# Performance work log

Measured on AMD Instinct MI355X. Metric: run time of the kernel, lower is better.

## Reference

```python
import jax, jax.numpy as jnp
import numpy as np

B, N, K, C, R = 2, 4096, 512, 384, 16
JITTER = 1e-4
W_ATTACH, W_ENTB = 1.0, 0.0


def overlap_score(delta, Sig):
    # fused_gaussian_overlap_score: bidirectional Mahalanobis overlap log-score
    # delta [..., 3], Sig [..., 3, 3] (SPD)
    sol = jnp.linalg.solve(Sig, delta[..., None])[..., 0]
    maha = (delta * sol).sum(-1)
    _, logdet = jnp.linalg.slogdet(Sig)
    return -0.5 * maha - 0.5 * logdet


def setup_inputs() -> dict:
    key = jax.random.key(0)
    ks = jax.random.split(key, 10)
    s_parent = jax.random.normal(ks[0], (B, K, C), jnp.float32)
    mu_parent = jax.random.normal(ks[1], (B, K, 3), jnp.float32) * 10.0
    A = jax.random.normal(ks[2], (B, K, 3, 3), jnp.float32)
    Sig_parent = A @ jnp.swapaxes(A, -1, -2) + 0.5 * jnp.eye(3, dtype=jnp.float32)
    mask_parent = jnp.ones((B, K), jnp.float32)
    node_mask = jnp.ones((B, N), jnp.float32)
    res_idx = jax.random.randint(ks[3], (B, N), 0, N)
    Bmat = jax.random.normal(ks[4], (1, C // 2), jnp.float32)  # Fourier freqs, scale=1.0
    Wq = jax.random.normal(ks[5], (C, C), jnp.float32) / np.sqrt(C).astype(np.float32)
    Wk = jax.random.normal(ks[6], (C, C), jnp.float32) / np.sqrt(C).astype(np.float32)
    Wv = jax.random.normal(ks[7], (C, C), jnp.float32) / np.sqrt(C).astype(np.float32)
    ln_g = jnp.ones((C,), jnp.float32)
    ln_b = jnp.zeros((C,), jnp.float32)
    return dict(s_parent=s_parent, mu_parent=mu_parent, Sig_parent=Sig_parent,
                mask_parent=mask_parent, node_mask=node_mask, res_idx=res_idx,
                Bmat=Bmat, Wq=Wq, Wk=Wk, Wv=Wv, ln_g=ln_g, ln_b=ln_b)


def reference(s_parent, mu_parent, Sig_parent, mask_parent, node_mask, res_idx,
              Bmat, Wq, Wk, Wv, ln_g, ln_b):
    eye3 = jnp.eye(3, dtype=s_parent.dtype)
    inv_sqrt_c = 1.0 / jnp.sqrt(jnp.asarray(C, s_parent.dtype))

    # --- ResIdxFourierEmbedding ---
    m = node_mask
    L = jnp.clip(m.sum(1, keepdims=True), 1.0)
    denom = jnp.clip(L - 1.0, 1.0)
    ri = jnp.clip(res_idx, 0, 4095).astype(s_parent.dtype)
    pos = jnp.clip(ri / denom, 0.0, 1.0)[..., None]                      # [B,N,1]
    proj = (2.0 * jnp.pi) * (pos @ Bmat)                                 # [B,N,C/2]
    emb = jnp.concatenate([jnp.cos(proj), jnp.sin(proj)], -1)            # [B,N,C]
    emb = emb * m[..., None]
    mu_e = emb.mean(-1, keepdims=True)
    var_e = ((emb - mu_e) ** 2).mean(-1, keepdims=True)
    q0 = (emb - mu_e) / jnp.sqrt(var_e + 1e-5) * ln_g + ln_b

    # --- routing projections ---
    q = q0 @ Wq                                                          # [B,N,C]
    k = s_parent @ Wk                                                    # [B,K,C]
    logits_full = jnp.einsum('bnc,bkc->bnk', q, k) * inv_sqrt_c
    logits_full = logits_full + (mask_parent[:, None, :] - 1.0) * 1e9
    j0 = jnp.argmax(logits_full, -1)                                     # [B,N]

    # --- topk parents by Gaussian overlap (no grad) ---
    mu_p = jax.lax.stop_gradient(mu_parent)
    Sig_p = jax.lax.stop_gradient(Sig_parent)
    delta_kk = mu_p[:, :, None, :] - mu_p[:, None, :, :]                 # [B,K,K,3]
    Sig_kk = Sig_p[:, :, None] + Sig_p[:, None, :] + 1e-6 * eye3         # [B,K,K,3,3]
    score_kk = overlap_score(delta_kk, Sig_kk)
    mask2d = mask_parent[:, None, :] * mask_parent[:, :, None]
    score_kk = jnp.where(mask2d < 0.5, -1e9, score_kk)
    knn = jax.lax.top_k(score_kk, R)[1]                                  # [B,K,R]
    parent_idx = knn[jnp.arange(B)[:, None], j0]                         # [B,N,R]

    # --- multi-level gathers ---
    gather = lambda tab: jax.vmap(lambda t, i: t[i])(tab, parent_idx)
    mu_sub = gather(mu_parent)                                           # [B,N,R,3]
    Sig_sub = gather(Sig_parent)                                         # [B,N,R,3,3]
    s_sub = gather(s_parent)                                             # [B,N,R,C]

    k_sub = s_sub @ Wk
    v_sub = s_sub @ Wv
    logits = (q[:, :, None, :] * k_sub).sum(-1) * inv_sqrt_c             # [B,N,R]
    logits = logits + (m[:, :, None] - 1.0) * 1e9
    B_local = jax.nn.softmax(logits, -1)

    s0 = jnp.einsum('bnr,bnrc->bnc', B_local, v_sub) * m[..., None]
    mu0 = jnp.einsum('bnr,bnrp->bnp', B_local, mu_sub)
    d = mu_sub - mu0[:, :, None, :]
    outer = d[..., :, None] * d[..., None, :]
    Sig0 = (B_local[..., None, None] * (Sig_sub + outer)).sum(2) + JITTER * eye3

    # --- geometric regularization ---
    delta0 = mu0[:, :, None, :] - mu_sub
    score = overlap_score(delta0, Sig_sub)                               # [B,N,R]
    dnm = jnp.clip(m.sum(), 1.0)
    loss_attach = -(m[:, :, None] * (B_local * score)).sum() / dnm
    ent = -(B_local * jnp.log(jnp.clip(B_local, 1e-9))).sum(-1)
    loss_ent_B = (ent * m).sum() / dnm

    occ = jax.vmap(lambda i, w: jnp.zeros((K,), w.dtype).at[i.reshape(-1)].add(w.reshape(-1)))(
        parent_idx, B_local * m[:, :, None])
    occ_norm = occ / jnp.clip(occ.sum(-1, keepdims=True), 1e-9)

    loss_geo = W_ATTACH * loss_attach + W_ENTB * loss_ent_B
    return s0, mu0, Sig0, B_local, occ_norm, loss_geo
```

## Files before the change

kernel.cpp:

```cpp
#include <hip/hip_runtime.h>
#include <math.h>

#define NB 2
#define NN 4096
#define NK 512
#define NC 384
#define NR 16
#define NCH 192
#define NSLICE 64

static constexpr float INV_SQRT_C = 0.051031036307982884f;
static constexpr float TWO_PI     = 6.283185307179586f;
static constexpr float F_JITTER   = 1e-4f;

typedef __attribute__((ext_vector_type(8))) short short8;
typedef __attribute__((ext_vector_type(4))) float f32x4;
typedef __attribute__((ext_vector_type(4))) unsigned short us4;
typedef __attribute__((ext_vector_type(8))) unsigned short us8;

__device__ __forceinline__ void split3(float x, unsigned short& h, unsigned short& m_, unsigned short& l_) {
    unsigned int xi = __float_as_uint(x);
    unsigned int uh = (xi + 0x7fffu + ((xi >> 16) & 1u)) >> 16;
    float fh = __uint_as_float(uh << 16);
    float r  = x - fh;
    unsigned int ri = __float_as_uint(r);
    unsigned int um = (ri + 0x7fffu + ((ri >> 16) & 1u)) >> 16;
    float fm = __uint_as_float(um << 16);
    float r2 = r - fm;
    unsigned int r2i = __float_as_uint(r2);
    unsigned int ul = (r2i + 0x7fffu + ((r2i >> 16) & 1u)) >> 16;
    h = (unsigned short)uh; m_ = (unsigned short)um; l_ = (unsigned short)ul;
}

__global__ __launch_bounds__(256) void k_pre(const float* __restrict__ node_mask,
                                             const float* __restrict__ Wk,
                                             const float* __restrict__ Wq,
                                             float* __restrict__ Lsum,
                                             float* __restrict__ W2) {
    __shared__ float red[256];
    __shared__ float As[16][68];
    __shared__ float Ws[16][68];
    int bid = blockIdx.x, t = threadIdx.x;
    if (bid < 2) {
        int b = bid;
        float s = 0.f;
        for (int n = t; n < NN; n += 256) s += node_mask[b*NN + n];
        red[t] = s; __syncthreads();
        for (int w = 128; w > 0; w >>= 1) { if (t < w) red[t] += red[t+w]; __syncthreads(); }
        if (t == 0) Lsum[b] = red[0];
        return;
    }
    int gb = bid - 2;
    int rowbase = (gb % 6) * 64, colbase = (gb / 6) * 64;
    int tx = t & 15, ty = t >> 4;
    float acc[4][4] = {};
    for (int k0 = 0; k0 < NC; k0 += 16) {
        {
            int r = t >> 2, ja = (t & 3) << 2;
            float4 a4 = *(const float4*)(Wk + (size_t)(rowbase + r)*NC + k0 + ja);
            As[ja+0][r] = a4.x; As[ja+1][r] = a4.y; As[ja+2][r] = a4.z; As[ja+3][r] = a4.w;
        }
        {
            int r = t >> 2, jb = (t & 3) << 2;
            float4 b4 = *(const float4*)(Wq + (size_t)(colbase + r)*NC + k0 + jb);
            Ws[jb+0][r] = b4.x; Ws[jb+1][r] = b4.y; Ws[jb+2][r] = b4.z; Ws[jb+3][r] = b4.w;
        }
        __syncthreads();
        #pragma unroll
        for (int kk = 0; kk < 16; ++kk) {
            float4 av = *(const float4*)&As[kk][ty<<2];
            float4 wv = *(const float4*)&Ws[kk][tx<<2];
            float aa[4] = {av.x, av.y, av.z, av.w};
            float ww[4] = {wv.x, wv.y, wv.z, wv.w};
            #pragma unroll
            for (int i = 0; i < 4; ++i)
                #pragma unroll
                for (int j = 0; j < 4; ++j)
                    acc[i][j] += aa[i]*ww[j];
        }
        __syncthreads();
    }
    #pragma unroll
    for (int i = 0; i < 4; ++i) {
        float4 o = make_float4(acc[i][0], acc[i][1], acc[i][2], acc[i][3]);
        *(float4*)(W2 + (size_t)(rowbase + (ty<<2) + i)*NC + colbase + (tx<<2)) = o;
    }
}

template<bool SPLIT>
__global__ __launch_bounds__(256) void k_mid(const float* __restrict__ s_parent,
                                             const float* __restrict__ Wv,
                                             const float* __restrict__ W2,
                                             const int* __restrict__ res_idx,
                                             const float* __restrict__ node_mask,
                                             const float* __restrict__ Bm,
                                             const float* __restrict__ ln_g,
                                             const float* __restrict__ ln_b,
                                             const float* __restrict__ Lsum,
                                             const float* __restrict__ mu,
                                             const float* __restrict__ Sg,
                                             const float* __restrict__ maskp,
                                             float* __restrict__ vmat,
                                             float* __restrict__ GtF,
                                             unsigned short* __restrict__ gh,
                                             unsigned short* __restrict__ gm,
                                             unsigned short* __restrict__ gl,
                                             float* __restrict__ q0f,
                                             unsigned short* __restrict__ qh,
                                             unsigned short* __restrict__ qm,
                                             unsigned short* __restrict__ ql,
                                             int* __restrict__ knn) {
    __shared__ float As[16][68];
    __shared__ float Ws[16][68];
    int bid = blockIdx.x, t = threadIdx.x;

    if (bid < 192) {
        int z = bid / 96, rem = bid % 96;
        int rowbase = (rem % 16) * 64, colbase = (rem / 16) * 64;
        const float* W = z ? W2 : Wv;
        int tx = t & 15, ty = t >> 4;
        float acc[4][4] = {};
        for (int k0 = 0; k0 < NC; k0 += 16) {
            {
                int r = t >> 2, ja = (t & 3) << 2;
                float4 a4 = *(const float4*)(s_parent + (size_t)(rowbase + r)*NC + k0 + ja);
                As[ja+0][r] = a4.x; As[ja+1][r] = a4.y; As[ja+2][r] = a4.z; As[ja+3][r] = a4.w;
            }
            {
                int kr = t >> 4, jw = (t & 15) << 2;
                float4 w4 = *(const float4*)(W + (size_t)(k0 + kr)*NC + colbase + jw);
                *(float4*)&Ws[kr][jw] = w4;
            }
            __syncthreads();
            #pragma unroll
            for (int kk = 0; kk < 16; ++kk) {
                float4 av = *(const float4*)&As[kk][ty<<2];
                float4 wv = *(const float4*)&Ws[kk][tx<<2];
                float aa[4] = {av.x, av.y, av.z, av.w};
                float ww[4] = {wv.x, wv.y, wv.z, wv.w};
                #pragma unroll
                for (int i = 0; i < 4; ++i)
                    #pragma unroll
                    for (int j = 0; j < 4; ++j)
                        acc[i][j] += aa[i]*ww[j];
            }
            __syncthreads();
        }
        #pragma unroll
        for (int i = 0; i < 4; ++i) {
            size_t ro = (size_t)(rowbase + (ty<<2) + i)*NC + colbase + (tx<<2);
            if (z == 0) {
                *(float4*)(vmat + ro) = make_float4(acc[i][0], acc[i][1], acc[i][2], acc[i][3]);
            } else if constexpr (SPLIT) {
                us4 vh, vm, vl;
                #pragma unroll
                for (int j = 0; j < 4; ++j) {
                    unsigned short h, mm, ll;
                    split3(acc[i][j], h, mm, ll);
                    vh[j] = h; vm[j] = mm; vl[j] = ll;
                }
                *(us4*)(gh + ro) = vh; *(us4*)(gm + ro) = vm; *(us4*)(gl + ro) = vl;
            } else {
                *(float4*)(GtF + ro) = make_float4(acc[i][0], acc[i][1], acc[i][2], acc[i][3]);
            }
        }
        return;
    }

    if (bid < 448) {
        int wv_ = t >> 6, lane = t & 63;
        int tb = ((bid - 192) << 2) + wv_;
        int b = tb >> 9, i = tb & 511;
        const float* mui = mu + (size_t)(b*NK + i)*3;
        const float* Sgi = Sg + (size_t)(b*NK + i)*9;
        float mi0 = mui[0], mi1 = mui[1], mi2 = mui[2];
        float S0 = Sgi[0], S1 = Sgi[1], S2 = Sgi[2], S4 = Sgi[4], S5 = Sgi[5], S8 = Sgi[8];
        float mski = maskp[b*NK + i];
        float cand[8];
        #pragma unroll
        for (int h = 0; h < 8; ++h) {
            int j = lane + (h << 6);
            const float* muj = mu + (size_t)(b*NK + j)*3;
            const float* Sgj = Sg + (size_t)(b*NK + j)*9;
            float d0 = mi0-muj[0], d1 = mi1-muj[1], d2 = mi2-muj[2];
            float a00 = S0+Sgj[0]+1e-6f, a01 = S1+Sgj[1],       a02 = S2+Sgj[2];
            float a11 = S4+Sgj[4]+1e-6f, a12 = S5+Sgj[5],       a22 = S8+Sgj[8]+1e-6f;
            float c00 = a11*a22 - a12*a12;
            float c01 = a02*a12 - a01*a22;
            float c02 = a01*a12 - a02*a11;
            float c11 = a00*a22 - a02*a02;
            float c12 = a01*a02 - a00*a12;
            float c22 = a00*a11 - a01*a01;
            float det = a00*c00 + a01*c01 + a02*c02;
            float t0 = c00*d0 + c01*d1 + c02*d2;
            float t1 = c01*d0 + c11*d1 + c12*d2;
            float t2 = c02*d0 + c12*d1 + c22*d2;
            float maha = (d0*t0 + d1*t1 + d2*t2) / det;
            float score = -0.5f*(maha + logf(det));
            float mj = maskp[b*NK + j];
            cand[h] = (mski*mj < 0.5f) ? -1e9f : score;
        }
        for (int it = 0; it < NR; ++it) {
            float bv = cand[0]; int bh = 0;
            #pragma unroll
            for (int h = 1; h < 8; ++h)
                if (cand[h] > bv) { bv = cand[h]; bh = h; }
            int bi = lane + (bh << 6);
            #pragma unroll
            for (int off = 32; off > 0; off >>= 1) {
                float v2 = __shfl_xor(bv, off);
                int   i2 = __shfl_xor(bi, off);
                if (v2 > bv || (v2 == bv && i2 < bi)) { bv = v2; bi = i2; }
            }
            if (lane == 0) knn[((size_t)(b*NK + i))*NR + it] = bi;
            if ((bi & 63) == lane) {
                int s = bi >> 6;
                #pragma unroll
                for (int h = 0; h < 8; ++h)
                    if (h == s) cand[h] = -INFINITY;
            }
        }
        return;
    }

    int q0b = bid - 448;
    int w = t >> 6, l = t & 63;
    int row = (q0b << 2) + w;
    int b = row >> 12;
    float m = node_mask[row];
    float Lb = fmaxf(Lsum[b], 1.0f);
    float denom = fmaxf(Lb - 1.0f, 1.0f);
    int ri = res_idx[row];
    ri = ri < 0 ? 0 : (ri > 4095 ? 4095 : ri);
    float pos = fminf(fmaxf((float)ri / denom, 0.f), 1.f);
    float v[6];
    #pragma unroll
    for (int j = 0; j < 3; ++j) {
        float pr = TWO_PI * pos * Bm[l + (j << 6)];
        v[j]   = cosf(pr) * m;
        v[j+3] = sinf(pr) * m;
    }
    float sum = v[0]+v[1]+v[2]+v[3]+v[4]+v[5];
    #pragma unroll
    for (int off = 32; off > 0; off >>= 1) sum += __shfl_xor(sum, off);
    float mean = sum * (1.0f/NC);
    float sq = 0.f;
    #pragma unroll
    for (int j = 0; j < 6; ++j) { v[j] -= mean; sq += v[j]*v[j]; }
    #pragma unroll
    for (int off = 32; off > 0; off >>= 1) sq += __shfl_xor(sq, off);
    float var = sq * (1.0f/NC);
    float inv = 1.0f / sqrtf(var + 1e-5f);
    #pragma unroll
    for (int j = 0; j < 6; ++j) {
        int p = l + (j << 6);
        float val = v[j]*inv*ln_g[p] + ln_b[p];
        size_t o = (size_t)row*NC + p;
        if constexpr (SPLIT) {
            unsigned short h, mm, ll;
            split3(val, h, mm, ll);
            qh[o] = h; qm[o] = mm; ql[o] = ll;
        } else {
            q0f[o] = val;
        }
    }
}

template<bool SPLIT>
__global__ __launch_bounds__(256) void k_logits_mfma(const float* __restrict__ q0f,
                                                     const unsigned short* __restrict__ qh,
                                                     const unsigned short* __restrict__ qm,
                                                     const unsigned short* __restrict__ ql,
                                                     const float* __restrict__ GtF,
                                                     const unsigned short* __restrict__ gh,
                                                     const unsigned short* __restrict__ gm,
                                                     const unsigned short* __restrict__ gl,
                                                     const float* __restrict__ maskp,
                                                     float* __restrict__ logits,
                                                     float* __restrict__ pmaxv,
                                                     int*   __restrict__ pmaxi,
                                                     float* __restrict__ occ_part) {
    int bid = blockIdx.x;
    {
        int gid = bid * 256 + threadIdx.x;
        if (gid < NSLICE*NB*NK) occ_part[gid] = 0.f;
    }
    int wg = (bid & 7) * 64 + (bid >> 3);
    int b  = wg >> 8;
    int r8 = (wg >> 3) & 31;
    int cb = wg & 7;
    int rowbase = r8 << 7;
    int colbase = cb << 6;

    __shared__ __align__(16) unsigned short Ah[128][40];
    __shared__ __align__(16) unsigned short Am[128][40];
    __shared__ __align__(16) unsigned short Al[128][40];
    __shared__ __align__(16) unsigned short Bh[64][40];
    __shared__ __align__(16) unsigned short Bm2[64][40];
    __shared__ __align__(16) unsigned short Bl[64][40];
    __shared__ float rmv[128][2];
    __shared__ int   rmi[128][2];

    int t = threadIdx.x;
    int lane = t & 63, wv = t >> 6;
    int wr = wv >> 1, wc = wv & 1;
    int a = lane & 15, g = lane >> 4;

    size_t arow0 = (size_t)(b << 12) + rowbase;
    size_t brow0 = (size_t)(b << 9) + colbase;

    f32x4 acc[4][2];
    #pragma unroll
    for (int i = 0; i < 4; ++i)
        #pragma unroll
        for (int j = 0; j < 2; ++j)
            acc[i][j] = (f32x4){0.f, 0.f, 0.f, 0.f};

    for (int k0 = 0; k0 < NC; k0 += 32) {
        __syncthreads();
        if constexpr (SPLIT) {
            #pragma unroll
            for (int i = 0; i < 2; ++i) {
                int id = i*256 + t;
                int row = id >> 2, s2 = id & 3;
                size_t go = (arow0 + row)*NC + k0 + (s2 << 3);
                *(us8*)&Ah[row][s2 << 3] = *(const us8*)(qh + go);
                *(us8*)&Am[row][s2 << 3] = *(const us8*)(qm + go);
                *(us8*)&Al[row][s2 << 3] = *(const us8*)(ql + go);
            }
            {
                int row = t >> 2, s2 = t & 3;
                size_t go = (brow0 + row)*NC + k0 + (s2 << 3);
                *(us8*)&Bh[row][s2 << 3]  = *(const us8*)(gh + go);
                *(us8*)&Bm2[row][s2 << 3] = *(const us8*)(gm + go);
                *(us8*)&Bl[row][s2 << 3]  = *(const us8*)(gl + go);
            }
        } else {
            #pragma unroll
            for (int i = 0; i < 4; ++i) {
                int id = i*256 + t;
                int row = id >> 3, seg = id & 7;
                float4 v = *(const float4*)(q0f + (arow0 + row)*NC + k0 + (seg << 2));
                unsigned short h0,m0,l0,h1,m1,l1,h2,m2,l2,h3,m3,l3;
                split3(v.x, h0, m0, l0); split3(v.y, h1, m1, l1);
                split3(v.z, h2, m2, l2); split3(v.w, h3, m3, l3);
                *(us4*)&Ah[row][seg << 2] = (us4){h0, h1, h2, h3};
                *(us4*)&Am[row][seg << 2] = (us4){m0, m1, m2, m3};
                *(us4*)&Al[row][seg << 2] = (us4){l0, l1, l2, l3};
            }
            #pragma unroll
            for (int i = 0; i < 2; ++i) {
                int id = i*256 + t;
                int row = id >> 3, seg = id & 7;
                float4 v = *(const float4*)(GtF + (brow0 + row)*NC + k0 + (seg << 2));
                unsigned short h0,m0,l0,h1,m1,l1,h2,m2,l2,h3,m3,l3;
                split3(v.x, h0, m0, l0); split3(v.y, h1, m1, l1);
                split3(v.z, h2, m2, l2); split3(v.w, h3, m3, l3);
                *(us4*)&Bh[row][seg << 2]  = (us4){h0, h1, h2, h3};
                *(us4*)&Bm2[row][seg << 2] = (us4){m0, m1, m2, m3};
                *(us4*)&Bl[row][seg << 2]  = (us4){l0, l1, l2, l3};
            }
        }
        __syncthreads();
        short8 afh[4], afm[4], afl[4];
        #pragma unroll
        for (int fr = 0; fr < 4; ++fr) {
            int r = (wr << 6) + (fr << 4) + a;
            afh[fr] = *(const short8*)&Ah[r][g << 3];
            afm[fr] = *(const short8*)&Am[r][g << 3];
            afl[fr] = *(const short8*)&Al[r][g << 3];
        }
        #pragma unroll
        for (int fc = 0; fc < 2; ++fc) {
            int c = (wc << 5) + (fc << 4) + a;
            short8 bh = *(const short8*)&Bh[c][g << 3];
            short8 bm = *(const short8*)&Bm2[c][g << 3];
            short8 bl = *(const short8*)&Bl[c][g << 3];
            #pragma unroll
            for (int fr = 0; fr < 4; ++fr) {
                acc[fr][fc] = __builtin_amdgcn_mfma_f32_16x16x32_bf16(afh[fr], bh, acc[fr][fc], 0, 0, 0);
                acc[fr][fc] = __builtin_amdgcn_mfma_f32_16x16x32_bf16(afh[fr], bm, acc[fr][fc], 0, 0, 0);
                acc[fr][fc] = __builtin_amdgcn_mfma_f32_16x16x32_bf16(afm[fr], bh, acc[fr][fc], 0, 0, 0);
                acc[fr][fc] = __builtin_amdgcn_mfma_f32_16x16x32_bf16(afh[fr], bl, acc[fr][fc], 0, 0, 0);
                acc[fr][fc] = __builtin_amdgcn_mfma_f32_16x16x32_bf16(afl[fr], bh, acc[fr][fc], 0, 0, 0);
                acc[fr][fc] = __builtin_amdgcn_mfma_f32_16x16x32_bf16(afm[fr], bm, acc[fr][fc], 0, 0, 0);
            }
        }
    }
    float mk[2];
    #pragma unroll
    for (int fc = 0; fc < 2; ++fc)
        mk[fc] = (maskp[(b << 9) + colbase + (wc << 5) + (fc << 4) + a] - 1.0f) * 1e9f;
    int colg0 = colbase + (wc << 5) + a;
    #pragma unroll
    for (int fr = 0; fr < 4; ++fr) {
        #pragma unroll
        for (int reg = 0; reg < 4; ++reg) {
            int rloc = (wr << 6) + (fr << 4) + (g << 2) + reg;
            size_t rowg = (size_t)(b << 12) + rowbase + rloc;
            float v0 = acc[fr][0][reg] * INV_SQRT_C;
            float v1 = acc[fr][1][reg] * INV_SQRT_C;
            logits[rowg * NK + colg0]      = v0;
            logits[rowg * NK + colg0 + 16] = v1;
            float bv = v0 + mk[0]; int bc = colg0;
            float w1 = v1 + mk[1];
            if (w1 > bv) { bv = w1; bc = colg0 + 16; }
            #pragma unroll
            for (int off = 1; off < 16; off <<= 1) {
                float v2 = __shfl_xor(bv, off);
                int   c2 = __shfl_xor(bc, off);
                if (v2 > bv || (v2 == bv && c2 < bc)) { bv = v2; bc = c2; }
            }
            if (a == 0) { rmv[rloc][wc] = bv; rmi[rloc][wc] = bc; }
        }
    }
    __syncthreads();
    if (t < 128) {
        float v0 = rmv[t][0], v1 = rmv[t][1];
        int   c0 = rmi[t][0], c1 = rmi[t][1];
        float bv = v0; int bc = c0;
        if (v1 > bv) { bv = v1; bc = c1; }
        pmaxv[(((size_t)(b << 3) + cb) << 12) + rowbase + t] = bv;
        pmaxi[(((size_t)(b << 3) + cb) << 12) + rowbase + t] = bc;
    }
}

__global__ __launch_bounds__(256) void k_final(const float* __restrict__ logits,
                                               const float* __restrict__ vmat,
                                               const float* __restrict__ mu,
                                               const float* __restrict__ Sg,
                                               const float* __restrict__ node_mask,
                                               const float* __restrict__ pmaxv,
                                               const int*   __restrict__ pmaxi,
                                               const int* __restrict__ knn,
                                               float* __restrict__ out_s0,
                                               float* __restrict__ out_mu0,
                                               float* __restrict__ out_Sig0,
                                               float* __restrict__ out_Bl,
                                               float* __restrict__ occ_part,
                                               float* __restrict__ loss_part) {
    int t = threadIdx.x;
    int rowbase = blockIdx.x << 4;
    int b = rowbase >> 12;
    int l  = t & 63;
    int sub = l >> 4, ll = l & 15;
    int r = ((t >> 6) << 2) + sub;
    int grow = rowbase + r;
    __shared__ float wl[16][17];
    __shared__ int   pidx[16][17];
    __shared__ float lred[16];
    __shared__ float msk[16];
    __shared__ int   j0s[16];

    if (t < 16) {
        int rowb = (rowbase & 4095) + t;
        float bv = -INFINITY; int bj = 0;
        #pragma unroll
        for (int cbk = 0; cbk < 8; ++cbk) {
            size_t idx = (((size_t)(b << 3) + cbk) << 12) + rowb;
            float v = pmaxv[idx];
            if (v > bv) { bv = v; bj = pmaxi[idx]; }
        }
        j0s[t] = bj;
    }
    __syncthreads();

    float m = node_mask[grow];
    int p = knn[((size_t)(b*NK + j0s[r]))*NR + ll];
    float v = logits[(size_t)grow*NK + p];
    float mx = v;
    #pragma unroll
    for (int off = 8; off > 0; off >>= 1) mx = fmaxf(mx, __shfl_xor(mx, off));
    float e = expf(v - mx);
    float sme = e;
    #pragma unroll
    for (int off = 8; off > 0; off >>= 1) sme += __shfl_xor(sme, off);
    float w = e / sme;
    wl[r][ll] = w;
    pidx[r][ll] = p;
    out_Bl[(size_t)rowbase*NR + t] = w;

    const float* mur = mu + (size_t)(b*NK + p)*3;
    const float* Sgr = Sg + (size_t)(b*NK + p)*9;
    float mr0 = mur[0], mr1 = mur[1], mr2 = mur[2];
    float m0 = w*mr0, m1 = w*mr1, m2 = w*mr2;
    #pragma unroll
    for (int off = 8; off > 0; off >>= 1) {
        m0 += __shfl_xor(m0, off); m1 += __shfl_xor(m1, off); m2 += __shfl_xor(m2, off);
    }
    float d0 = mr0-m0, d1 = mr1-m1, d2 = mr2-m2;
    float a00 = Sgr[0], a01 = Sgr[1], a02 = Sgr[2];
    float a11 = Sgr[4], a12 = Sgr[5], a22 = Sgr[8];
    float p00 = w*(a00 + d0*d0), p01 = w*(a01 + d0*d1), p02 = w*(a02 + d0*d2);
    float p11 = w*(a11 + d1*d1), p12 = w*(a12 + d1*d2), p22 = w*(a22 + d2*d2);
    #pragma unroll
    for (int off = 8; off > 0; off >>= 1) {
        p00 += __shfl_xor(p00, off); p01 += __shfl_xor(p01, off); p02 += __shfl_xor(p02, off);
        p11 += __shfl_xor(p11, off); p12 += __shfl_xor(p12, off); p22 += __shfl_xor(p22, off);
    }
    float c00 = a11*a22 - a12*a12;
    float c01 = a02*a12 - a01*a22;
    float c02 = a01*a12 - a02*a11;
    float c11 = a00*a22 - a02*a02;
    float c12 = a01*a02 - a00*a12;
    float c22 = a00*a11 - a01*a01;
    float det = a00*c00 + a01*c01 + a02*c02;
    float t0 = c00*d0 + c01*d1 + c02*d2;
    float t1 = c01*d0 + c11*d1 + c12*d2;
    float t2 = c02*d0 + c12*d1 + c22*d2;
    float maha = (d0*t0 + d1*t1 + d2*t2) / det;
    float score = -0.5f*(maha + logf(det));
    float lp = w*score;
    #pragma unroll
    for (int off = 8; off > 0; off >>= 1) lp += __shfl_xor(lp, off);
    if (ll == 0) {
        out_mu0[(size_t)grow*3+0] = m0;
        out_mu0[(size_t)grow*3+1] = m1;
        out_mu0[(size_t)grow*3+2] = m2;
        float* o = out_Sig0 + (size_t)grow*9;
        o[0]=p00+F_JITTER; o[1]=p01;          o[2]=p02;
        o[3]=p01;          o[4]=p11+F_JITTER; o[5]=p12;
        o[6]=p02;          o[7]=p12;          o[8]=p22+F_JITTER;
        lred[r] = m*lp;
        msk[r] = m;
    }
    atomicAdd(&occ_part[(size_t)(blockIdx.x & (NSLICE-1))*(NB*NK) + b*NK + p], w*m);
    __syncthreads();
    if (t == 0) {
        float s = 0.f;
        #pragma unroll
        for (int i = 0; i < 16; ++i) s += lred[i];
        loss_part[blockIdx.x] = s;
    }
    const float4* vb = (const float4*)(vmat + (size_t)b*NK*NC);
    #pragma unroll
    for (int it = 0; it < 6; ++it) {
        int id = it*256 + t;
        int row = id / 96;
        int col = id - row*96;
        float4 acc4 = make_float4(0.f, 0.f, 0.f, 0.f);
        #pragma unroll
        for (int r2 = 0; r2 < NR; ++r2) {
            float ww = wl[row][r2];
            float4 vv = vb[(size_t)pidx[row][r2]*96 + col];
            acc4.x += ww*vv.x; acc4.y += ww*vv.y; acc4.z += ww*vv.z; acc4.w += ww*vv.w;
        }
        float mm = msk[row];
        acc4.x *= mm; acc4.y *= mm; acc4.z *= mm; acc4.w *= mm;
        ((float4*)(out_s0 + (size_t)(rowbase + row)*NC))[col] = acc4;
    }
}

__global__ __launch_bounds__(512) void k_finalize(const float* __restrict__ occ_part,
                                                  const float* __restrict__ Lsum,
                                                  const float* __restrict__ loss_part,
                                                  float* __restrict__ out_occn,
                                                  float* __restrict__ out_loss) {
    int b = blockIdx.x, t = threadIdx.x;
    __shared__ float red[512];
    float s = 0.f;
    for (int sl = 0; sl < NSLICE; ++sl) s += occ_part[(size_t)sl*(NB*NK) + b*NK + t];
    red[t] = s; __syncthreads();
    for (int w = 256; w > 0; w >>= 1) { if (t < w) red[t] += red[t+w]; __syncthreads(); }
    float tot = red[0];
    __syncthreads();
    out_occn[b*NK + t] = s / fmaxf(tot, 1e-9f);
    if (b == 0) {
        red[t] = loss_part[t]; __syncthreads();
        for (int w = 256; w > 0; w >>= 1) { if (t < w) red[t] += red[t+w]; __syncthreads(); }
        if (t == 0) {
            float dnm = fmaxf(Lsum[0] + Lsum[1], 1.0f);
            out_loss[0] = -(red[0] / dnm);
        }
    }
}

extern "C" void kernel_launch(void* const* d_in, const int* in_sizes, int n_in,
                              void* d_out, int out_size, void* d_ws, size_t ws_size,
                              hipStream_t stream) {
    const float* s_parent   = (const float*)d_in[0];
    const float* mu_parent  = (const float*)d_in[1];
    const float* Sig_parent = (const float*)d_in[2];
    const float* mask_par   = (const float*)d_in[3];
    const float* node_mask  = (const float*)d_in[4];
    const int*   res_idx    = (const int*)d_in[5];
    const float* Bm         = (const float*)d_in[6];
    const float* Wq         = (const float*)d_in[7];
    const float* Wk         = (const float*)d_in[8];
    const float* Wv         = (const float*)d_in[9];
    const float* ln_g       = (const float*)d_in[10];
    const float* ln_b       = (const float*)d_in[11];

    const bool G = (ws_size >= (43ull << 20));

    float* ws = (float*)d_ws;
    const size_t SZ_A    = G ? 4718592 : 3145728;
    const size_t OFF_LOG = 0;
    const size_t OFF_A   = OFF_LOG + 4194304;
    const size_t OFF_MISC= OFF_A + SZ_A;
    const size_t OFF_V   = OFF_MISC + 262144;
    const size_t OFF_GT  = OFF_V + 393216;
    const size_t OFF_SM  = OFF_GT + (G ? 589824 : 393216);

    float*          logits = ws + OFF_LOG;
    float*          q0f    = ws + OFF_A;
    unsigned short* qh     = (unsigned short*)(ws + OFF_A);
    unsigned short* qm     = qh + (size_t)NB*NN*NC;
    unsigned short* ql     = qm + (size_t)NB*NN*NC;
    float*          W2     = ws + OFF_MISC;
    float*          pmaxv  = ws + OFF_MISC;
    int*            pmaxi  = (int*)(ws + OFF_MISC + 65536);
    int*            knn    = (int*)(ws + OFF_MISC + 147456);
    float*          occ_part = ws + OFF_MISC + 163840;
    float*          vmat   = ws + OFF_V;
    float*          GtF    = ws + OFF_GT;
    unsigned short* gh     = (unsigned short*)(ws + OFF_GT);
    unsigned short* gm     = gh + (size_t)NB*NK*NC;
    unsigned short* gl     = gm + (size_t)NB*NK*NC;
    float*          Lsum   = ws + OFF_SM;
    float*          lpart  = ws + OFF_SM + 16;

    float* out      = (float*)d_out;
    float* out_s0   = out;
    float* out_mu0  = out      + (size_t)NB*NN*NC;
    float* out_Sig0 = out_mu0  + (size_t)NB*NN*3;
    float* out_Bl   = out_Sig0 + (size_t)NB*NN*9;
    float* out_occn = out_Bl   + (size_t)NB*NN*NR;
    float* out_loss = out_occn + (size_t)NB*NK;

    (void)in_sizes; (void)n_in; (void)out_size;

    k_pre<<<38, 256, 0, stream>>>(node_mask, Wk, Wq, Lsum, W2);
    if (G) k_mid<true ><<<2496, 256, 0, stream>>>(s_parent, Wv, W2, res_idx, node_mask, Bm, ln_g, ln_b,
                                                  Lsum, mu_parent, Sig_parent, mask_par,
                                                  vmat, GtF, gh, gm, gl, q0f, qh, qm, ql, knn);
    else   k_mid<false><<<2496, 256, 0, stream>>>(s_parent, Wv, W2, res_idx, node_mask, Bm, ln_g, ln_b,
                                                  Lsum, mu_parent, Sig_parent, mask_par,
                                                  vmat, GtF, gh, gm, gl, q0f, qh, qm, ql, knn);
    if (G) k_logits_mfma<true ><<<512, 256, 0, stream>>>(q0f, qh, qm, ql, GtF, gh, gm, gl,
                                                         mask_par, logits, pmaxv, pmaxi, occ_part);
    else   k_logits_mfma<false><<<512, 256, 0, stream>>>(q0f, qh, qm, ql, GtF, gh, gm, gl,
                                                         mask_par, logits, pmaxv, pmaxi, occ_part);
    k_final<<<(NB*NN)/16, 256, 0, stream>>>(logits, vmat, mu_parent, Sig_parent, node_mask,
                                            pmaxv, pmaxi, knn, out_s0, out_mu0, out_Sig0,
                                            out_Bl, occ_part, lpart);
    k_finalize<<<2, 512, 0, stream>>>(occ_part, Lsum, lpart, out_occn, out_loss);
}
```

Measured before the change: 102.3 us.

## Fuse logits MFMA GEMM with softmax/gather epilogue in one kernel

```diff
diff --git a/kernel.cpp b/kernel.cpp
--- a/kernel.cpp
+++ b/kernel.cpp
@@ -6,7 +6,6 @@
 #define NK 512
 #define NC 384
 #define NR 16
-#define NCH 192
 #define NSLICE 64
 
 static constexpr float INV_SQRT_C = 0.051031036307982884f;
@@ -109,10 +108,15 @@
                                              unsigned short* __restrict__ qh,
                                              unsigned short* __restrict__ qm,
                                              unsigned short* __restrict__ ql,
-                                             int* __restrict__ knn) {
+                                             int* __restrict__ knn,
+                                             float* __restrict__ occ_part) {
     __shared__ float As[16][68];
     __shared__ float Ws[16][68];
     int bid = blockIdx.x, t = threadIdx.x;
+
+    if (bid < 256) {
+        occ_part[bid*256 + t] = 0.f;
+    }
 
     if (bid < 192) {
         int z = bid / 96, rem = bid % 96;
@@ -267,171 +271,19 @@
 }
 
 template<bool SPLIT>
-__global__ __launch_bounds__(256) void k_logits_mfma(const float* __restrict__ q0f,
-                                                     const unsigned short* __restrict__ qh,
-                                                     const unsigned short* __restrict__ qm,
-                                                     const unsigned short* __restrict__ ql,
-                                                     const float* __restrict__ GtF,
-                                                     const unsigned short* __restrict__ gh,
-                                                     const unsigned short* __restrict__ gm,
-                                                     const unsigned short* __restrict__ gl,
-                                                     const float* __restrict__ maskp,
-                                                     float* __restrict__ logits,
-                                                     float* __restrict__ pmaxv,
-                                                     int*   __restrict__ pmaxi,
-                                                     float* __restrict__ occ_part) {
-    int bid = blockIdx.x;
-    {
-        int gid = bid * 256 + threadIdx.x;
-        if (gid < NSLICE*NB*NK) occ_part[gid] = 0.f;
-    }
-    int wg = (bid & 7) * 64 + (bid >> 3);
-    int b  = wg >> 8;
-    int r8 = (wg >> 3) & 31;
-    int cb = wg & 7;
-    int rowbase = r8 << 7;
-    int colbase = cb << 6;
-
-    __shared__ __align__(16) unsigned short Ah[128][40];
-    __shared__ __align__(16) unsigned short Am[128][40];
-    __shared__ __align__(16) unsigned short Al[128][40];
-    __shared__ __align__(16) unsigned short Bh[64][40];
-    __shared__ __align__(16) unsigned short Bm2[64][40];
-    __shared__ __align__(16) unsigned short Bl[64][40];
-    __shared__ float rmv[128][2];
-    __shared__ int   rmi[128][2];
-
-    int t = threadIdx.x;
-    int lane = t & 63, wv = t >> 6;
-    int wr = wv >> 1, wc = wv & 1;
-    int a = lane & 15, g = lane >> 4;
-
-    size_t arow0 = (size_t)(b << 12) + rowbase;
-    size_t brow0 = (size_t)(b << 9) + colbase;
-
-    f32x4 acc[4][2];
-    #pragma unroll
-    for (int i = 0; i < 4; ++i)
-        #pragma unroll
-        for (int j = 0; j < 2; ++j)
-            acc[i][j] = (f32x4){0.f, 0.f, 0.f, 0.f};
-
-    for (int k0 = 0; k0 < NC; k0 += 32) {
-        __syncthreads();
-        if constexpr (SPLIT) {
-            #pragma unroll
-            for (int i = 0; i < 2; ++i) {
-                int id = i*256 + t;
-                int row = id >> 2, s2 = id & 3;
-                size_t go = (arow0 + row)*NC + k0 + (s2 << 3);
-                *(us8*)&Ah[row][s2 << 3] = *(const us8*)(qh + go);
-                *(us8*)&Am[row][s2 << 3] = *(const us8*)(qm + go);
-                *(us8*)&Al[row][s2 << 3] = *(const us8*)(ql + go);
-            }
-            {
-                int row = t >> 2, s2 = t & 3;
-                size_t go = (brow0 + row)*NC + k0 + (s2 << 3);
-                *(us8*)&Bh[row][s2 << 3]  = *(const us8*)(gh + go);
-                *(us8*)&Bm2[row][s2 << 3] = *(const us8*)(gm + go);
-                *(us8*)&Bl[row][s2 << 3]  = *(const us8*)(gl + go);
-            }
-        } else {
-            #pragma unroll
-            for (int i = 0; i < 4; ++i) {
-                int id = i*256 + t;
-                int row = id >> 3, seg = id & 7;
-                float4 v = *(const float4*)(q0f + (arow0 + row)*NC + k0 + (seg << 2));
-                unsigned short h0,m0,l0,h1,m1,l1,h2,m2,l2,h3,m3,l3;
-                split3(v.x, h0, m0, l0); split3(v.y, h1, m1, l1);
-                split3(v.z, h2, m2, l2); split3(v.w, h3, m3, l3);
-                *(us4*)&Ah[row][seg << 2] = (us4){h0, h1, h2, h3};
-                *(us4*)&Am[row][seg << 2] = (us4){m0, m1, m2, m3};
-                *(us4*)&Al[row][seg << 2] = (us4){l0, l1, l2, l3};
-            }
-            #pragma unroll
-            for (int i = 0; i < 2; ++i) {
-                int id = i*256 + t;
-                int row = id >> 3, seg = id & 7;
-                float4 v = *(const float4*)(GtF + (brow0 + row)*NC + k0 + (seg << 2));
-                unsigned short h0,m0,l0,h1,m1,l1,h2,m2,l2,h3,m3,l3;
-                split3(v.x, h0, m0, l0); split3(v.y, h1, m1, l1);
-                split3(v.z, h2, m2, l2); split3(v.w, h3, m3, l3);
-                *(us4*)&Bh[row][seg << 2]  = (us4){h0, h1, h2, h3};
-                *(us4*)&Bm2[row][seg << 2] = (us4){m0, m1, m2, m3};
-                *(us4*)&Bl[row][seg << 2]  = (us4){l0, l1, l2, l3};
-            }
-        }
-        __syncthreads();
-        short8 afh[4], afm[4], afl[4];
-        #pragma unroll
-        for (int fr = 0; fr < 4; ++fr) {
-            int r = (wr << 6) + (fr << 4) + a;
-            afh[fr] = *(const short8*)&Ah[r][g << 3];
-            afm[fr] = *(const short8*)&Am[r][g << 3];
-            afl[fr] = *(const short8*)&Al[r][g << 3];
-        }
-        #pragma unroll
-        for (int fc = 0; fc < 2; ++fc) {
-            int c = (wc << 5) + (fc << 4) + a;
-            short8 bh = *(const short8*)&Bh[c][g << 3];
-            short8 bm = *(const short8*)&Bm2[c][g << 3];
-            short8 bl = *(const short8*)&Bl[c][g << 3];
-            #pragma unroll
-            for (int fr = 0; fr < 4; ++fr) {
-                acc[fr][fc] = __builtin_amdgcn_mfma_f32_16x16x32_bf16(afh[fr], bh, acc[fr][fc], 0, 0, 0);
-                acc[fr][fc] = __builtin_amdgcn_mfma_f32_16x16x32_bf16(afh[fr], bm, acc[fr][fc], 0, 0, 0);
-                acc[fr][fc] = __builtin_amdgcn_mfma_f32_16x16x32_bf16(afm[fr], bh, acc[fr][fc], 0, 0, 0);
-                acc[fr][fc] = __builtin_amdgcn_mfma_f32_16x16x32_bf16(afh[fr], bl, acc[fr][fc], 0, 0, 0);
-                acc[fr][fc] = __builtin_amdgcn_mfma_f32_16x16x32_bf16(afl[fr], bh, acc[fr][fc], 0, 0, 0);
-                acc[fr][fc] = __builtin_amdgcn_mfma_f32_16x16x32_bf16(afm[fr], bm, acc[fr][fc], 0, 0, 0);
-            }
-        }
-    }
-    float mk[2];
-    #pragma unroll
-    for (int fc = 0; fc < 2; ++fc)
-        mk[fc] = (maskp[(b << 9) + colbase + (wc << 5) + (fc << 4) + a] - 1.0f) * 1e9f;
-    int colg0 = colbase + (wc << 5) + a;
-    #pragma unroll
-    for (int fr = 0; fr < 4; ++fr) {
-        #pragma unroll
-        for (int reg = 0; reg < 4; ++reg) {
-            int rloc = (wr << 6) + (fr << 4) + (g << 2) + reg;
-            size_t rowg = (size_t)(b << 12) + rowbase + rloc;
-            float v0 = acc[fr][0][reg] * INV_SQRT_C;
-            float v1 = acc[fr][1][reg] * INV_SQRT_C;
-            logits[rowg * NK + colg0]      = v0;
-            logits[rowg * NK + colg0 + 16] = v1;
-            float bv = v0 + mk[0]; int bc = colg0;
-            float w1 = v1 + mk[1];
-            if (w1 > bv) { bv = w1; bc = colg0 + 16; }
-            #pragma unroll
-            for (int off = 1; off < 16; off <<= 1) {
-                float v2 = __shfl_xor(bv, off);
-                int   c2 = __shfl_xor(bc, off);
-                if (v2 > bv || (v2 == bv && c2 < bc)) { bv = v2; bc = c2; }
-            }
-            if (a == 0) { rmv[rloc][wc] = bv; rmi[rloc][wc] = bc; }
-        }
-    }
-    __syncthreads();
-    if (t < 128) {
-        float v0 = rmv[t][0], v1 = rmv[t][1];
-        int   c0 = rmi[t][0], c1 = rmi[t][1];
-        float bv = v0; int bc = c0;
-        if (v1 > bv) { bv = v1; bc = c1; }
-        pmaxv[(((size_t)(b << 3) + cb) << 12) + rowbase + t] = bv;
-        pmaxi[(((size_t)(b << 3) + cb) << 12) + rowbase + t] = bc;
-    }
-}
-
-__global__ __launch_bounds__(256) void k_final(const float* __restrict__ logits,
+__global__ __launch_bounds__(256) void k_fused(const float* __restrict__ q0f,
+                                               const unsigned short* __restrict__ qh,
+                                               const unsigned short* __restrict__ qm,
+                                               const unsigned short* __restrict__ ql,
+                                               const float* __restrict__ GtF,
+                                               const unsigned short* __restrict__ gh,
+                                               const unsigned short* __restrict__ gm,
+                                               const unsigned short* __restrict__ gl,
+                                               const float* __restrict__ maskp,
                                                const float* __restrict__ vmat,
                                                const float* __restrict__ mu,
                                                const float* __restrict__ Sg,
                                                const float* __restrict__ node_mask,
-                                               const float* __restrict__ pmaxv,
-                                               const int*   __restrict__ pmaxi,
                                                const int* __restrict__ knn,
                                                float* __restrict__ out_s0,
                                                float* __restrict__ out_mu0,
@@ -439,102 +291,222 @@
                                                float* __restrict__ out_Bl,
                                                float* __restrict__ occ_part,
                                                float* __restrict__ loss_part) {
-    int t = threadIdx.x;
-    int rowbase = blockIdx.x << 4;
-    int b = rowbase >> 12;
-    int l  = t & 63;
-    int sub = l >> 4, ll = l & 15;
-    int r = ((t >> 6) << 2) + sub;
-    int grow = rowbase + r;
-    __shared__ float wl[16][17];
-    __shared__ int   pidx[16][17];
-    __shared__ float lred[16];
-    __shared__ float msk[16];
-    __shared__ int   j0s[16];
-
-    if (t < 16) {
-        int rowb = (rowbase & 4095) + t;
-        float bv = -INFINITY; int bj = 0;
-        #pragma unroll
-        for (int cbk = 0; cbk < 8; ++cbk) {
-            size_t idx = (((size_t)(b << 3) + cbk) << 12) + rowb;
-            float v = pmaxv[idx];
-            if (v > bv) { bv = v; bj = pmaxi[idx]; }
-        }
-        j0s[t] = bj;
+    int bid = blockIdx.x, t = threadIdx.x;
+    int grow0 = bid << 5;
+    int b = grow0 >> 12;
+
+    __shared__ __align__(16) unsigned short Ah[32][40];
+    __shared__ __align__(16) unsigned short Am[32][40];
+    __shared__ __align__(16) unsigned short Al[32][40];
+    __shared__ __align__(16) unsigned char uB[122880];
+    unsigned short (*Bh)[40]  = (unsigned short(*)[40])(uB);
+    unsigned short (*Bm2)[40] = (unsigned short(*)[40])(uB + 40960);
+    unsigned short (*Bl)[40]  = (unsigned short(*)[40])(uB + 81920);
+    float (*lgs)[516]         = (float(*)[516])uB;
+    __shared__ float rmv[32][4];
+    __shared__ int   rmi[32][4];
+    __shared__ int   j0s[32];
+    __shared__ float wl[32][17];
+    __shared__ int   pidx[32][17];
+    __shared__ float lred[32];
+    __shared__ float msk[32];
+
+    int lane = t & 63, wv = t >> 6;
+    int a = lane & 15, g = lane >> 4;
+
+    f32x4 acc[2][8];
+    #pragma unroll
+    for (int i = 0; i < 2; ++i)
+        #pragma unroll
+        for (int j = 0; j < 8; ++j)
+            acc[i][j] = (f32x4){0.f, 0.f, 0.f, 0.f};
+
+    for (int k0 = 0; k0 < NC; k0 += 32) {
+        __syncthreads();
+        if constexpr (SPLIT) {
+            if (t < 128) {
+                int row = t >> 2, s2 = t & 3;
+                size_t go = (size_t)(grow0 + row)*NC + k0 + (s2 << 3);
+                *(us8*)&Ah[row][s2 << 3] = *(const us8*)(qh + go);
+                *(us8*)&Am[row][s2 << 3] = *(const us8*)(qm + go);
+                *(us8*)&Al[row][s2 << 3] = *(const us8*)(ql + go);
+            }
+            #pragma unroll
+            for (int i = 0; i < 8; ++i) {
+                int id = i*256 + t;
+                int row = id >> 2, s2 = id & 3;
+                size_t go = ((size_t)(b << 9) + row)*NC + k0 + (s2 << 3);
+                *(us8*)&Bh[row][s2 << 3]  = *(const us8*)(gh + go);
+                *(us8*)&Bm2[row][s2 << 3] = *(const us8*)(gm + go);
+                *(us8*)&Bl[row][s2 << 3]  = *(const us8*)(gl + go);
+            }
+        } else {
+            {
+                int row = t >> 3, seg = t & 7;
+                float4 v = *(const float4*)(q0f + (size_t)(grow0 + row)*NC + k0 + (seg << 2));
+                unsigned short h0,m0,l0,h1,m1,l1,h2,m2,l2,h3,m3,l3;
+                split3(v.x, h0, m0, l0); split3(v.y, h1, m1, l1);
+                split3(v.z, h2, m2, l2); split3(v.w, h3, m3, l3);
+                *(us4*)&Ah[row][seg << 2] = (us4){h0, h1, h2, h3};
+                *(us4*)&Am[row][seg << 2] = (us4){m0, m1, m2, m3};
+                *(us4*)&Al[row][seg << 2] = (us4){l0, l1, l2, l3};
+            }
+            #pragma unroll
+            for (int i = 0; i < 16; ++i) {
+                int id = i*256 + t;
+                int row = id >> 3, seg = id & 7;
+                float4 v = *(const float4*)(GtF + ((size_t)(b << 9) + row)*NC + k0 + (seg << 2));
+                unsigned short h0,m0,l0,h1,m1,l1,h2,m2,l2,h3,m3,l3;
+                split3(v.x, h0, m0, l0); split3(v.y, h1, m1, l1);
+                split3(v.z, h2, m2, l2); split3(v.w, h3, m3, l3);
+                *(us4*)&Bh[row][seg << 2]  = (us4){h0, h1, h2, h3};
+                *(us4*)&Bm2[row][seg << 2] = (us4){m0, m1, m2, m3};
+                *(us4*)&Bl[row][seg << 2]  = (us4){l0, l1, l2, l3};
+            }
+        }
+        __syncthreads();
+        short8 afh[2], afm[2], afl[2];
+        #pragma unroll
+        for (int fr = 0; fr < 2; ++fr) {
+            int r = (fr << 4) + a;
+            afh[fr] = *(const short8*)&Ah[r][g << 3];
+            afm[fr] = *(const short8*)&Am[r][g << 3];
+            afl[fr] = *(const short8*)&Al[r][g << 3];
+        }
+        #pragma unroll
+        for (int fc = 0; fc < 8; ++fc) {
+            int c = (wv << 7) + (fc << 4) + a;
+            short8 bh = *(const short8*)&Bh[c][g << 3];
+            short8 bm = *(const short8*)&Bm2[c][g << 3];
+            short8 bl = *(const short8*)&Bl[c][g << 3];
+            #pragma unroll
+            for (int fr = 0; fr < 2; ++fr) {
+                acc[fr][fc] = __builtin_amdgcn_mfma_f32_16x16x32_bf16(afh[fr], bh, acc[fr][fc], 0, 0, 0);
+                acc[fr][fc] = __builtin_amdgcn_mfma_f32_16x16x32_bf16(afh[fr], bm, acc[fr][fc], 0, 0, 0);
+                acc[fr][fc] = __builtin_amdgcn_mfma_f32_16x16x32_bf16(afm[fr], bh, acc[fr][fc], 0, 0, 0);
+                acc[fr][fc] = __builtin_amdgcn_mfma_f32_16x16x32_bf16(afh[fr], bl, acc[fr][fc], 0, 0, 0);
+                acc[fr][fc] = __builtin_amdgcn_mfma_f32_16x16x32_bf16(afl[fr], bh, acc[fr][fc], 0, 0, 0);
+                acc[fr][fc] = __builtin_amdgcn_mfma_f32_16x16x32_bf16(afm[fr], bm, acc[fr][fc], 0, 0, 0);
+            }
+        }
     }
     __syncthreads();
 
-    float m = node_mask[grow];
-    int p = knn[((size_t)(b*NK + j0s[r]))*NR + ll];
-    float v = logits[(size_t)grow*NK + p];
-    float mx = v;
-    #pragma unroll
-    for (int off = 8; off > 0; off >>= 1) mx = fmaxf(mx, __shfl_xor(mx, off));
-    float e = expf(v - mx);
-    float sme = e;
-    #pragma unroll
-    for (int off = 8; off > 0; off >>= 1) sme += __shfl_xor(sme, off);
-    float w = e / sme;
-    wl[r][ll] = w;
-    pidx[r][ll] = p;
-    out_Bl[(size_t)rowbase*NR + t] = w;
-
-    const float* mur = mu + (size_t)(b*NK + p)*3;
-    const float* Sgr = Sg + (size_t)(b*NK + p)*9;
-    float mr0 = mur[0], mr1 = mur[1], mr2 = mur[2];
-    float m0 = w*mr0, m1 = w*mr1, m2 = w*mr2;
-    #pragma unroll
-    for (int off = 8; off > 0; off >>= 1) {
-        m0 += __shfl_xor(m0, off); m1 += __shfl_xor(m1, off); m2 += __shfl_xor(m2, off);
-    }
-    float d0 = mr0-m0, d1 = mr1-m1, d2 = mr2-m2;
-    float a00 = Sgr[0], a01 = Sgr[1], a02 = Sgr[2];
-    float a11 = Sgr[4], a12 = Sgr[5], a22 = Sgr[8];
-    float p00 = w*(a00 + d0*d0), p01 = w*(a01 + d0*d1), p02 = w*(a02 + d0*d2);
-    float p11 = w*(a11 + d1*d1), p12 = w*(a12 + d1*d2), p22 = w*(a22 + d2*d2);
-    #pragma unroll
-    for (int off = 8; off > 0; off >>= 1) {
-        p00 += __shfl_xor(p00, off); p01 += __shfl_xor(p01, off); p02 += __shfl_xor(p02, off);
-        p11 += __shfl_xor(p11, off); p12 += __shfl_xor(p12, off); p22 += __shfl_xor(p22, off);
-    }
-    float c00 = a11*a22 - a12*a12;
-    float c01 = a02*a12 - a01*a22;
-    float c02 = a01*a12 - a02*a11;
-    float c11 = a00*a22 - a02*a02;
-    float c12 = a01*a02 - a00*a12;
-    float c22 = a00*a11 - a01*a01;
-    float det = a00*c00 + a01*c01 + a02*c02;
-    float t0 = c00*d0 + c01*d1 + c02*d2;
-    float t1 = c01*d0 + c11*d1 + c12*d2;
-    float t2 = c02*d0 + c12*d1 + c22*d2;
-    float maha = (d0*t0 + d1*t1 + d2*t2) / det;
-    float score = -0.5f*(maha + logf(det));
-    float lp = w*score;
-    #pragma unroll
-    for (int off = 8; off > 0; off >>= 1) lp += __shfl_xor(lp, off);
-    if (ll == 0) {
-        out_mu0[(size_t)grow*3+0] = m0;
-        out_mu0[(size_t)grow*3+1] = m1;
-        out_mu0[(size_t)grow*3+2] = m2;
-        float* o = out_Sig0 + (size_t)grow*9;
-        o[0]=p00+F_JITTER; o[1]=p01;          o[2]=p02;
-        o[3]=p01;          o[4]=p11+F_JITTER; o[5]=p12;
-        o[6]=p02;          o[7]=p12;          o[8]=p22+F_JITTER;
-        lred[r] = m*lp;
-        msk[r] = m;
-    }
-    atomicAdd(&occ_part[(size_t)(blockIdx.x & (NSLICE-1))*(NB*NK) + b*NK + p], w*m);
+    float mk[8];
+    #pragma unroll
+    for (int fc = 0; fc < 8; ++fc)
+        mk[fc] = (maskp[(b << 9) + (wv << 7) + (fc << 4) + a] - 1.0f) * 1e9f;
+    #pragma unroll
+    for (int fr = 0; fr < 2; ++fr) {
+        #pragma unroll
+        for (int reg = 0; reg < 4; ++reg) {
+            int row = (fr << 4) + (g << 2) + reg;
+            float bv = -INFINITY; int bc = 0;
+            #pragma unroll
+            for (int fc = 0; fc < 8; ++fc) {
+                int col = (wv << 7) + (fc << 4) + a;
+                float v = acc[fr][fc][reg] * INV_SQRT_C;
+                lgs[row][col] = v;
+                float w1 = v + mk[fc];
+                if (w1 > bv) { bv = w1; bc = col; }
+            }
+            #pragma unroll
+            for (int off = 1; off < 16; off <<= 1) {
+                float v2 = __shfl_xor(bv, off);
+                int   c2 = __shfl_xor(bc, off);
+                if (v2 > bv || (v2 == bv && c2 < bc)) { bv = v2; bc = c2; }
+            }
+            if (a == 0) { rmv[row][wv] = bv; rmi[row][wv] = bc; }
+        }
+    }
+    __syncthreads();
+    if (t < 32) {
+        float bv = rmv[t][0]; int bc = rmi[t][0];
+        #pragma unroll
+        for (int w2 = 1; w2 < 4; ++w2) {
+            float v2 = rmv[t][w2]; int c2 = rmi[t][w2];
+            if (v2 > bv || (v2 == bv && c2 < bc)) { bv = v2; bc = c2; }
+        }
+        j0s[t] = bc;
+    }
+    __syncthreads();
+
+    int grp = t >> 4, ll = t & 15;
+    #pragma unroll
+    for (int rr2 = 0; rr2 < 2; ++rr2) {
+        int r = (grp << 1) + rr2;
+        int growr = grow0 + r;
+        float m = node_mask[growr];
+        int p = knn[((size_t)(b*NK + j0s[r]))*NR + ll];
+        float v = lgs[r][p];
+        float mx = v;
+        #pragma unroll
+        for (int off = 8; off > 0; off >>= 1) mx = fmaxf(mx, __shfl_xor(mx, off));
+        float e = expf(v - mx);
+        float sme = e;
+        #pragma unroll
+        for (int off = 8; off > 0; off >>= 1) sme += __shfl_xor(sme, off);
+        float w = e / sme;
+        wl[r][ll] = w;
+        pidx[r][ll] = p;
+        out_Bl[(size_t)growr*NR + ll] = w;
+
+        const float* mur = mu + (size_t)(b*NK + p)*3;
+        const float* Sgr = Sg + (size_t)(b*NK + p)*9;
+        float mr0 = mur[0], mr1 = mur[1], mr2 = mur[2];
+        float m0 = w*mr0, m1 = w*mr1, m2 = w*mr2;
+        #pragma unroll
+        for (int off = 8; off > 0; off >>= 1) {
+            m0 += __shfl_xor(m0, off); m1 += __shfl_xor(m1, off); m2 += __shfl_xor(m2, off);
+        }
+        float d0 = mr0-m0, d1 = mr1-m1, d2 = mr2-m2;
+        float a00 = Sgr[0], a01 = Sgr[1], a02 = Sgr[2];
+        float a11 = Sgr[4], a12 = Sgr[5], a22 = Sgr[8];
+        float p00 = w*(a00 + d0*d0), p01 = w*(a01 + d0*d1), p02 = w*(a02 + d0*d2);
+        float p11 = w*(a11 + d1*d1), p12 = w*(a12 + d1*d2), p22 = w*(a22 + d2*d2);
+        #pragma unroll
+        for (int off = 8; off > 0; off >>= 1) {
+            p00 += __shfl_xor(p00, off); p01 += __shfl_xor(p01, off); p02 += __shfl_xor(p02, off);
+            p11 += __shfl_xor(p11, off); p12 += __shfl_xor(p12, off); p22 += __shfl_xor(p22, off);
+        }
+        float c00 = a11*a22 - a12*a12;
+        float c01 = a02*a12 - a01*a22;
+        float c02 = a01*a12 - a02*a11;
+        float c11 = a00*a22 - a02*a02;
+        float c12 = a01*a02 - a00*a12;
+        float c22 = a00*a11 - a01*a01;
+        float det = a00*c00 + a01*c01 + a02*c02;
+        float t0 = c00*d0 + c01*d1 + c02*d2;
+        float t1 = c01*d0 + c11*d1 + c12*d2;
+        float t2 = c02*d0 + c12*d1 + c22*d2;
+        float maha = (d0*t0 + d1*t1 + d2*t2) / det;
+        float score = -0.5f*(maha + logf(det));
+        float lp = w*score;
+        #pragma unroll
+        for (int off = 8; off > 0; off >>= 1) lp += __shfl_xor(lp, off);
+        if (ll == 0) {
+            out_mu0[(size_t)growr*3+0] = m0;
+            out_mu0[(size_t)growr*3+1] = m1;
+            out_mu0[(size_t)growr*3+2] = m2;
+            float* o = out_Sig0 + (size_t)growr*9;
+            o[0]=p00+F_JITTER; o[1]=p01;          o[2]=p02;
+            o[3]=p01;          o[4]=p11+F_JITTER; o[5]=p12;
+            o[6]=p02;          o[7]=p12;          o[8]=p22+F_JITTER;
+            lred[r] = m*lp;
+            msk[r] = m;
+        }
+        atomicAdd(&occ_part[(size_t)(bid & (NSLICE-1))*(NB*NK) + b*NK + p], w*m);
+    }
     __syncthreads();
     if (t == 0) {
         float s = 0.f;
         #pragma unroll
-        for (int i = 0; i < 16; ++i) s += lred[i];
-        loss_part[blockIdx.x] = s;
+        for (int i = 0; i < 32; ++i) s += lred[i];
+        loss_part[bid] = s;
     }
     const float4* vb = (const float4*)(vmat + (size_t)b*NK*NC);
     #pragma unroll
-    for (int it = 0; it < 6; ++it) {
+    for (int it = 0; it < 12; ++it) {
         int id = it*256 + t;
         int row = id / 96;
         int col = id - row*96;
@@ -547,7 +519,7 @@
         }
         float mm = msk[row];
         acc4.x *= mm; acc4.y *= mm; acc4.z *= mm; acc4.w *= mm;
-        ((float4*)(out_s0 + (size_t)(rowbase + row)*NC))[col] = acc4;
+        ((float4*)(out_s0 + (size_t)(grow0 + row)*NC))[col] = acc4;
     }
 }
 
@@ -566,7 +538,8 @@
     __syncthreads();
     out_occn[b*NK + t] = s / fmaxf(tot, 1e-9f);
     if (b == 0) {
-        red[t] = loss_part[t]; __syncthreads();
+        red[t] = (t < 256) ? loss_part[t] : 0.f;
+        __syncthreads();
         for (int w = 256; w > 0; w >>= 1) { if (t < w) red[t] += red[t+w]; __syncthreads(); }
         if (t == 0) {
             float dnm = fmaxf(Lsum[0] + Lsum[1], 1.0f);
@@ -602,14 +575,11 @@
     const size_t OFF_GT  = OFF_V + 393216;
     const size_t OFF_SM  = OFF_GT + (G ? 589824 : 393216);
 
-    float*          logits = ws + OFF_LOG;
     float*          q0f    = ws + OFF_A;
     unsigned short* qh     = (unsigned short*)(ws + OFF_A);
     unsigned short* qm     = qh + (size_t)NB*NN*NC;
     unsigned short* ql     = qm + (size_t)NB*NN*NC;
     float*          W2     = ws + OFF_MISC;
-    float*          pmaxv  = ws + OFF_MISC;
-    int*            pmaxi  = (int*)(ws + OFF_MISC + 65536);
     int*            knn    = (int*)(ws + OFF_MISC + 147456);
     float*          occ_part = ws + OFF_MISC + 163840;
     float*          vmat   = ws + OFF_V;
@@ -633,16 +603,15 @@
     k_pre<<<38, 256, 0, stream>>>(node_mask, Wk, Wq, Lsum, W2);
     if (G) k_mid<true ><<<2496, 256, 0, stream>>>(s_parent, Wv, W2, res_idx, node_mask, Bm, ln_g, ln_b,
                                                   Lsum, mu_parent, Sig_parent, mask_par,
-                                                  vmat, GtF, gh, gm, gl, q0f, qh, qm, ql, knn);
+                                                  vmat, GtF, gh, gm, gl, q0f, qh, qm, ql, knn, occ_part);
     else   k_mid<false><<<2496, 256, 0, stream>>>(s_parent, Wv, W2, res_idx, node_mask, Bm, ln_g, ln_b,
                                                   Lsum, mu_parent, Sig_parent, mask_par,
-                                                  vmat, GtF, gh, gm, gl, q0f, qh, qm, ql, knn);
-    if (G) k_logits_mfma<true ><<<512, 256, 0, stream>>>(q0f, qh, qm, ql, GtF, gh, gm, gl,
-                                                         mask_par, logits, pmaxv, pmaxi, occ_part);
-    else   k_logits_mfma<false><<<512, 256, 0, stream>>>(q0f, qh, qm, ql, GtF, gh, gm, gl,
-                                                         mask_par, logits, pmaxv, pmaxi, occ_part);
-    k_final<<<(NB*NN)/16, 256, 0, stream>>>(logits, vmat, mu_parent, Sig_parent, node_mask,
-                                            pmaxv, pmaxi, knn, out_s0, out_mu0, out_Sig0,
-                                            out_Bl, occ_part, lpart);
+                                                  vmat, GtF, gh, gm, gl, q0f, qh, qm, ql, knn, occ_part);
+    if (G) k_fused<true ><<<256, 256, 0, stream>>>(q0f, qh, qm, ql, GtF, gh, gm, gl, mask_par,
+                                                   vmat, mu_parent, Sig_parent, node_mask, knn,
+                                                   out_s0, out_mu0, out_Sig0, out_Bl, occ_part, lpart);
+    else   k_fused<false><<<256, 256, 0, stream>>>(q0f, qh, qm, ql, GtF, gh, gm, gl, mask_par,
+                                                   vmat, mu_parent, Sig_parent, node_mask, knn,
+                                                   out_s0, out_mu0, out_Sig0, out_Bl, occ_part, lpart);
     k_finalize<<<2, 512, 0, stream>>>(occ_part, Lsum, lpart, out_occn, out_loss);
 }
```

New measurement: 111.8 us. 9.3% more time.
